# Performance work log

Measured on AMD Instinct MI355X. Metric: run time of the kernel, lower is better.

The kernel has to match this reference:

```python
import jax, jax.numpy as jnp
import numpy as np

B, DEC, ENC, HID, UNITS = 4, 256, 1024, 512, 128


def setup_inputs() -> dict:
    key = jax.random.key(0)
    k1, k2, k3, k4, k5, k6 = jax.random.split(key, 6)
    query = jax.random.normal(k1, (B, DEC, HID), dtype=jnp.float32)
    value = jax.random.normal(k2, (B, ENC, HID), dtype=jnp.float32)
    mask = jax.random.bernoulli(k3, 0.9, (B, ENC))  # bool, True = keep
    # Dense(units, use_bias=False) kernels, glorot-ish scaling
    W1 = jax.random.normal(k4, (HID, UNITS), dtype=jnp.float32) * (1.0 / np.sqrt(HID))
    W2 = jax.random.normal(k5, (HID, UNITS), dtype=jnp.float32) * (1.0 / np.sqrt(HID))
    # AdditiveAttention use_scale=True: learned per-unit scale vector
    scale = jax.random.normal(k6, (UNITS,), dtype=jnp.float32) * (1.0 / np.sqrt(UNITS))
    return {"query": query, "value": value, "mask": mask, "W1": W1, "W2": W2, "scale": scale}


def reference(query, value, mask, W1, W2, scale):
    # query: (B, DEC, HID), value: (B, ENC, HID), mask: (B, ENC) bool
    q = jnp.einsum("bqh,hu->bqu", query, W1)   # (B, DEC, U)
    k = jnp.einsum("beh,hu->beu", value, W2)   # (B, ENC, U)
    # Bahdanau additive score: sum_u scale_u * tanh(q + k)  -> (B, DEC, ENC)
    scores = jnp.einsum("bqeu,u->bqe", jnp.tanh(q[:, :, None, :] + k[:, None, :, :]), scale)
    neg = jnp.asarray(-1e9, scores.dtype)
    scores = jnp.where(mask[:, None, :], scores, neg)
    attention_weights = jax.nn.softmax(scores, axis=-1)   # (B, DEC, ENC)
    context_vector = jnp.einsum("bqe,beh->bqh", attention_weights, value)  # (B, DEC, HID)
    # query_mask is all-ones in the original module -> no-op on output
    return (context_vector, attention_weights)
```

## Files before the change

kernel.cpp:

```cpp
#include <hip/hip_runtime.h>
#include <cstddef>

#define B     4
#define DEC   256
#define ENC   1024
#define HID   512
#define UNITS 128

#define PROJ_SCALE 2.8853900817779268f

__global__ __launch_bounds__(256) void proj_kernel(
    const float* __restrict__ query, const float* __restrict__ value,
    const float* __restrict__ W1,    const float* __restrict__ W2,
    float* __restrict__ qbuf,        float* __restrict__ kbufT)
{
    __shared__ float xs[8][HID];
    __shared__ float part[4][8][UNITS];

    const int tid  = threadIdx.x;
    const int lane = tid & 63;
    const int wv   = __builtin_amdgcn_readfirstlane(tid >> 6);
    const int row0g = blockIdx.x * 8;
    const bool isQ = row0g < B * DEC;
    const float* X = isQ ? query : value;
    const float* W = isQ ? W1 : W2;
    const int row0 = isQ ? row0g : row0g - B * DEC;
    const int h0   = wv * 128;

    {
        const float* xb = X + (size_t)row0 * HID;
        #pragma unroll
        for (int k = 0; k < 4; ++k) {
            const float4 v = *(const float4*)(xb + (size_t)k * 1024 + tid * 4);
            *(float4*)&xs[0][k * 1024 + tid * 4] = v;
        }
    }
    __syncthreads();

    float acc0[8], acc1[8];
    #pragma unroll
    for (int r = 0; r < 8; ++r) { acc0[r] = 0.f; acc1[r] = 0.f; }

    const float* Wb = W + (size_t)h0 * UNITS + 2 * lane;

    float2 wcur[4], wnxt[4];
    #pragma unroll
    for (int j = 0; j < 4; ++j) wcur[j] = *(const float2*)(Wb + j * UNITS);
    #pragma unroll
    for (int j = 0; j < 4; ++j) wnxt[j] = *(const float2*)(Wb + (4 + j) * UNITS);

    for (int h = 0; h < 128; h += 4) {
        const int hp = (h + 8 < 128) ? h + 8 : h;
        float2 np[4];
        #pragma unroll
        for (int j = 0; j < 4; ++j)
            np[j] = *(const float2*)(Wb + (hp + j) * UNITS);

        #pragma unroll
        for (int r = 0; r < 8; ++r) {
            const float4 xv = *(const float4*)&xs[r][h0 + h];
            acc0[r] = fmaf(xv.x, wcur[0].x, acc0[r]);
            acc1[r] = fmaf(xv.x, wcur[0].y, acc1[r]);
            acc0[r] = fmaf(xv.y, wcur[1].x, acc0[r]);
            acc1[r] = fmaf(xv.y, wcur[1].y, acc1[r]);
            acc0[r] = fmaf(xv.z, wcur[2].x, acc0[r]);
            acc1[r] = fmaf(xv.z, wcur[2].y, acc1[r]);
            acc0[r] = fmaf(xv.w, wcur[3].x, acc0[r]);
            acc1[r] = fmaf(xv.w, wcur[3].y, acc1[r]);
        }
        #pragma unroll
        for (int j = 0; j < 4; ++j) { wcur[j] = wnxt[j]; wnxt[j] = np[j]; }
    }

    #pragma unroll
    for (int r = 0; r < 8; ++r)
        *(float2*)&part[wv][r][2 * lane] = make_float2(acc0[r], acc1[r]);
    __syncthreads();

    #pragma unroll
    for (int k = 0; k < 4; ++k) {
        const int idx = tid + k * 256;
        const int r = idx >> 7, u = idx & (UNITS - 1);
        const float s = PROJ_SCALE *
            ((part[0][r][u] + part[1][r][u]) + (part[2][r][u] + part[3][r][u]));
        const float z = __builtin_amdgcn_exp2f(s);
        const int row = row0 + r;
        if (isQ) {
            qbuf[(size_t)row * UNITS + u] = z;
        } else {
            const int bb = row >> 10, e = row & (ENC - 1);
            const int c = u >> 2, j = u & 3;
            kbufT[((size_t)bb * 32 * ENC + (size_t)c * ENC + e) * 4 + j] = z;
        }
    }
}

__device__ __forceinline__ float quad_term(const float4 q, const float4 k,
                                           const float4 s) {
    const float A  = fmaf(q.x, k.x, 1.f);
    const float B_ = fmaf(q.y, k.y, 1.f);
    const float C  = fmaf(q.z, k.z, 1.f);
    const float D  = fmaf(q.w, k.w, 1.f);
    const float AB = A * B_, CD = C * D;
    const float n1 = fmaf(s.x, B_, s.y * A);
    const float n2 = fmaf(s.z, D,  s.w * C);
    const float num = fmaf(n1, CD, n2 * AB);
    return num * __builtin_amdgcn_rcpf(AB * CD);
}

__global__ __launch_bounds__(1024) void score_kernel(
    const float* __restrict__ qbuf, const float* __restrict__ kbufT,
    const int* __restrict__ mask,   const float* __restrict__ scale,
    float* __restrict__ attn_out)
{
    const int bi  = blockIdx.x;
    const int b   = (bi >> 1) & 3;
    const int dq0 = (((bi >> 3) << 1) | (bi & 1)) * 4;
    const int tid = threadIdx.x;

    const int m = mask[b * ENC + tid];

    const float* q0 = qbuf + (size_t)(b * DEC + dq0) * UNITS;
    const float* kc = kbufT + (size_t)b * 32 * ENC * 4 + (size_t)tid * 4;

    float t0 = 0.f, t1 = 0.f, t2 = 0.f, t3 = 0.f;

    float4 kv = *(const float4*)kc;
    for (int i = 0; i < 32; ++i) {
        float4 nkv;
        if (i + 1 < 32) nkv = *(const float4*)(kc + (size_t)(i + 1) * ENC * 4);
        const float4 sv = *(const float4*)(scale + i * 4);
        const float4 qa = *(const float4*)(q0 + 0 * UNITS + i * 4);
        const float4 qb = *(const float4*)(q0 + 1 * UNITS + i * 4);
        const float4 qc = *(const float4*)(q0 + 2 * UNITS + i * 4);
        const float4 qd = *(const float4*)(q0 + 3 * UNITS + i * 4);

        t0 += quad_term(qa, kv, sv);
        t1 += quad_term(qb, kv, sv);
        t2 += quad_term(qc, kv, sv);
        t3 += quad_term(qd, kv, sv);

        if (i + 1 < 32) kv = nkv;
    }

    float wgt[4];
    wgt[0] = m ? __expf(-2.f * t0) : 0.f;
    wgt[1] = m ? __expf(-2.f * t1) : 0.f;
    wgt[2] = m ? __expf(-2.f * t2) : 0.f;
    wgt[3] = m ? __expf(-2.f * t3) : 0.f;

    __shared__ float reds[4][16];
    const int lane = tid & 63, wv = tid >> 6;

    float ls[4] = {wgt[0], wgt[1], wgt[2], wgt[3]};
    #pragma unroll
    for (int off = 32; off > 0; off >>= 1) {
        #pragma unroll
        for (int r = 0; r < 4; ++r)
            ls[r] += __shfl_down(ls[r], off, 64);
    }
    if (lane == 0) {
        #pragma unroll
        for (int r = 0; r < 4; ++r) reds[r][wv] = ls[r];
    }
    __syncthreads();
    #pragma unroll
    for (int r = 0; r < 4; ++r) {
        float g = 0.f;
        #pragma unroll
        for (int w = 0; w < 16; ++w) g += reds[r][w];
        attn_out[(size_t)(b * DEC + dq0 + r) * ENC + tid] =
            wgt[r] * __builtin_amdgcn_rcpf(g);
    }
}

__global__ __launch_bounds__(512) void ctx_kernel(
    const float* __restrict__ attn, const float* __restrict__ value,
    float* __restrict__ ctx)
{
    __shared__ float attnS[8][ENC];
    __shared__ float part[8][8][128];

    const int bi   = blockIdx.x;
    const int b    = (bi >> 1) & 3;
    const int idx  = ((bi >> 3) << 1) | (bi & 1);
    const int row0 = (idx >> 2) * 8;
    const int h0   = (idx & 3) * 128;
    const int tid  = threadIdx.x;
    const int lane = tid & 63;
    const int wv   = __builtin_amdgcn_readfirstlane(tid >> 6);

    const float* ab = attn + (size_t)(b * DEC + row0) * ENC;
    #pragma unroll
    for (int k = 0; k < 4; ++k) {
        const float4 v = *(const float4*)(ab + (size_t)k * 2048 + tid * 4);
        *(float4*)&attnS[0][k * 2048 + tid * 4] = v;
    }
    __syncthreads();

    float acc[8][2];
    #pragma unroll
    for (int r = 0; r < 8; ++r) { acc[r][0] = 0.f; acc[r][1] = 0.f; }

    const float* vb = value + (size_t)b * ENC * HID + h0 + lane * 2;
    const int e0 = wv * 128;

    float2 va[4];
    #pragma unroll
    for (int j = 0; j < 4; ++j)
        va[j] = *(const float2*)(vb + (size_t)(e0 + j) * HID);

    for (int g = 0; g < 32; ++g) {
        const int gp = (g + 1 < 32) ? g + 1 : g;
        float2 vn[4];
        #pragma unroll
        for (int j = 0; j < 4; ++j)
            vn[j] = *(const float2*)(vb + (size_t)(e0 + gp * 4 + j) * HID);

        const int eg = e0 + g * 4;
        float4 w4[8];
        #pragma unroll
        for (int r = 0; r < 8; ++r)
            w4[r] = *(const float4*)&attnS[r][eg];

        #pragma unroll
        for (int j = 0; j < 4; ++j) {
            const float2 v2 = va[j];
            #pragma unroll
            for (int r = 0; r < 8; ++r) {
                const float w = ((const float*)&w4[r])[j];
                acc[r][0] += w * v2.x;
                acc[r][1] += w * v2.y;
            }
        }
        #pragma unroll
        for (int j = 0; j < 4; ++j) va[j] = vn[j];
    }

    #pragma unroll
    for (int r = 0; r < 8; ++r)
        *(float2*)&part[wv][r][lane * 2] = make_float2(acc[r][0], acc[r][1]);
    __syncthreads();

    #pragma unroll
    for (int k = 0; k < 2; ++k) {
        const int idx2 = tid + k * 512;
        const int r = idx2 >> 7, hh = idx2 & 127;
        float s = 0.f;
        #pragma unroll
        for (int w = 0; w < 8; ++w) s += part[w][r][hh];
        ctx[(size_t)(b * DEC + row0 + r) * HID + h0 + hh] = s;
    }
}

extern "C" void kernel_launch(void* const* d_in, const int* in_sizes, int n_in,
                              void* d_out, int out_size, void* d_ws, size_t ws_size,
                              hipStream_t stream) {
    const float* query = (const float*)d_in[0];
    const float* value = (const float*)d_in[1];
    const int*   mask  = (const int*)  d_in[2];
    const float* W1    = (const float*)d_in[3];
    const float* W2    = (const float*)d_in[4];
    const float* scale = (const float*)d_in[5];

    float* qbuf  = (float*)d_ws;
    float* kbufT = qbuf + (size_t)B * DEC * UNITS;

    float* ctx_out  = (float*)d_out;
    float* attn_out = ctx_out + (size_t)B * DEC * HID;

    proj_kernel <<<640,  256, 0, stream>>>(query, value, W1, W2, qbuf, kbufT);
    score_kernel<<<256, 1024, 0, stream>>>(qbuf, kbufT, mask, scale, attn_out);
    ctx_kernel  <<<512,  512, 0, stream>>>(attn_out, value, ctx_out);
}
```

Measured before the change: 123.3 us.

## Fuse context matmul into score kernel, keeping normalized weights in shared memory

Merges the separate context kernel into the score kernel. Each 1024-thread block now multiplies its 4 normalized attention rows, held in shared memory, by the full value matrix across all 512 hidden columns. This removes one launch and the global re-read of the attention matrix. In exchange, each block streams the whole per-batch value slice (2 MB) for only 4 rows, so value reuse per block halves compared with 8 rows before. The block also uses more shared memory (about 48 KB), which may limit occupancy.

```diff
diff --git a/kernel.cpp b/kernel.cpp
--- a/kernel.cpp
+++ b/kernel.cpp
@@ -108,17 +108,31 @@
     return num * __builtin_amdgcn_rcpf(AB * CD);
 }
 
-__global__ __launch_bounds__(1024) void score_kernel(
+__global__ __launch_bounds__(1024) void score_ctx_kernel(
     const float* __restrict__ qbuf, const float* __restrict__ kbufT,
     const int* __restrict__ mask,   const float* __restrict__ scale,
-    float* __restrict__ attn_out)
+    const float* __restrict__ value,
+    float* __restrict__ attn_out,   float* __restrict__ ctx)
 {
+    __shared__ float wS[4][ENC];
+    __shared__ float part[4][4][HID];
+    __shared__ float reds[4][16];
+
     const int bi  = blockIdx.x;
     const int b   = (bi >> 1) & 3;
     const int dq0 = (((bi >> 3) << 1) | (bi & 1)) * 4;
     const int tid = threadIdx.x;
 
     const int m = mask[b * ENC + tid];
+
+    const int h2 = tid & 255;
+    const int eq = tid >> 8;
+    const float* vb2 = value + (size_t)b * ENC * HID
+                     + (size_t)(eq * 256) * HID + 2 * h2;
+    float2 va[4];
+    #pragma unroll
+    for (int j = 0; j < 4; ++j)
+        va[j] = *(const float2*)(vb2 + (size_t)j * HID);
 
     const float* q0 = qbuf + (size_t)(b * DEC + dq0) * UNITS;
     const float* kc = kbufT + (size_t)b * 32 * ENC * 4 + (size_t)tid * 4;
@@ -149,7 +163,6 @@
     wgt[2] = m ? __expf(-2.f * t2) : 0.f;
     wgt[3] = m ? __expf(-2.f * t3) : 0.f;
 
-    __shared__ float reds[4][16];
     const int lane = tid & 63, wv = tid >> 6;
 
     float ls[4] = {wgt[0], wgt[1], wgt[2], wgt[3]};
@@ -164,73 +177,43 @@
         for (int r = 0; r < 4; ++r) reds[r][wv] = ls[r];
     }
     __syncthreads();
+
     #pragma unroll
     for (int r = 0; r < 4; ++r) {
         float g = 0.f;
         #pragma unroll
         for (int w = 0; w < 16; ++w) g += reds[r][w];
-        attn_out[(size_t)(b * DEC + dq0 + r) * ENC + tid] =
-            wgt[r] * __builtin_amdgcn_rcpf(g);
-    }
-}
-
-__global__ __launch_bounds__(512) void ctx_kernel(
-    const float* __restrict__ attn, const float* __restrict__ value,
-    float* __restrict__ ctx)
-{
-    __shared__ float attnS[8][ENC];
-    __shared__ float part[8][8][128];
-
-    const int bi   = blockIdx.x;
-    const int b    = (bi >> 1) & 3;
-    const int idx  = ((bi >> 3) << 1) | (bi & 1);
-    const int row0 = (idx >> 2) * 8;
-    const int h0   = (idx & 3) * 128;
-    const int tid  = threadIdx.x;
-    const int lane = tid & 63;
-    const int wv   = __builtin_amdgcn_readfirstlane(tid >> 6);
-
-    const float* ab = attn + (size_t)(b * DEC + row0) * ENC;
-    #pragma unroll
-    for (int k = 0; k < 4; ++k) {
-        const float4 v = *(const float4*)(ab + (size_t)k * 2048 + tid * 4);
-        *(float4*)&attnS[0][k * 2048 + tid * 4] = v;
-    }
-    __syncthreads();
-
-    float acc[8][2];
-    #pragma unroll
-    for (int r = 0; r < 8; ++r) { acc[r][0] = 0.f; acc[r][1] = 0.f; }
-
-    const float* vb = value + (size_t)b * ENC * HID + h0 + lane * 2;
-    const int e0 = wv * 128;
-
-    float2 va[4];
-    #pragma unroll
-    for (int j = 0; j < 4; ++j)
-        va[j] = *(const float2*)(vb + (size_t)(e0 + j) * HID);
-
-    for (int g = 0; g < 32; ++g) {
-        const int gp = (g + 1 < 32) ? g + 1 : g;
+        const float wn = wgt[r] * __builtin_amdgcn_rcpf(g);
+        attn_out[(size_t)(b * DEC + dq0 + r) * ENC + tid] = wn;
+        wS[r][tid] = wn;
+    }
+    __syncthreads();
+
+    float2 acc[4];
+    #pragma unroll
+    for (int r = 0; r < 4; ++r) acc[r] = make_float2(0.f, 0.f);
+
+    for (int g = 0; g < 64; ++g) {
+        const int gp = (g + 1 < 64) ? g + 1 : g;
         float2 vn[4];
         #pragma unroll
         for (int j = 0; j < 4; ++j)
-            vn[j] = *(const float2*)(vb + (size_t)(e0 + gp * 4 + j) * HID);
-
-        const int eg = e0 + g * 4;
-        float4 w4[8];
-        #pragma unroll
-        for (int r = 0; r < 8; ++r)
-            w4[r] = *(const float4*)&attnS[r][eg];
+            vn[j] = *(const float2*)(vb2 + (size_t)(gp * 4 + j) * HID);
+
+        const int e = eq * 256 + g * 4;
+        float4 w4[4];
+        #pragma unroll
+        for (int r = 0; r < 4; ++r)
+            w4[r] = *(const float4*)&wS[r][e];
 
         #pragma unroll
         for (int j = 0; j < 4; ++j) {
             const float2 v2 = va[j];
             #pragma unroll
-            for (int r = 0; r < 8; ++r) {
+            for (int r = 0; r < 4; ++r) {
                 const float w = ((const float*)&w4[r])[j];
-                acc[r][0] += w * v2.x;
-                acc[r][1] += w * v2.y;
+                acc[r].x = fmaf(w, v2.x, acc[r].x);
+                acc[r].y = fmaf(w, v2.y, acc[r].y);
             }
         }
         #pragma unroll
@@ -238,18 +221,17 @@
     }
 
     #pragma unroll
-    for (int r = 0; r < 8; ++r)
-        *(float2*)&part[wv][r][lane * 2] = make_float2(acc[r][0], acc[r][1]);
+    for (int r = 0; r < 4; ++r)
+        *(float2*)&part[eq][r][2 * h2] = acc[r];
     __syncthreads();
 
     #pragma unroll
     for (int k = 0; k < 2; ++k) {
-        const int idx2 = tid + k * 512;
-        const int r = idx2 >> 7, hh = idx2 & 127;
-        float s = 0.f;
-        #pragma unroll
-        for (int w = 0; w < 8; ++w) s += part[w][r][hh];
-        ctx[(size_t)(b * DEC + row0 + r) * HID + h0 + hh] = s;
+        const int idx = tid + k * 1024;
+        const int r = idx >> 9, hh = idx & 511;
+        const float s = (part[0][r][hh] + part[1][r][hh])
+                      + (part[2][r][hh] + part[3][r][hh]);
+        ctx[(size_t)(b * DEC + dq0 + r) * HID + hh] = s;
     }
 }
 
@@ -269,7 +251,7 @@
     float* ctx_out  = (float*)d_out;
     float* attn_out = ctx_out + (size_t)B * DEC * HID;
 
-    proj_kernel <<<640,  256, 0, stream>>>(query, value, W1, W2, qbuf, kbufT);
-    score_kernel<<<256, 1024, 0, stream>>>(qbuf, kbufT, mask, scale, attn_out);
-    ctx_kernel  <<<512,  512, 0, stream>>>(attn_out, value, ctx_out);
-}
+    proj_kernel     <<<640,  256, 0, stream>>>(query, value, W1, W2, qbuf, kbufT);
+    score_ctx_kernel<<<256, 1024, 0, stream>>>(qbuf, kbufT, mask, scale, value,
+                                               attn_out, ctx_out);
+}
```

Result: slower. 133.9 us (+8.5%).
